# Kernel tuning notes

Hardware: AMD Instinct MI355X
Metric: run time of the kernel (lower is better)

Reference implementation:

```python
import jax, jax.numpy as jnp
import numpy as np

NUM_HEADS = 16
ROPE_THETA = 10000.0


def _rope(x, cos, sin):
    # x: [B, H, S, d_k]; cos/sin: [S, d_k//2]
    x2 = x.reshape(x.shape[:-1] + (x.shape[-1] // 2, 2))
    x0, x1 = x2[..., 0], x2[..., 1]
    out0 = cos * x0 - sin * x1
    out1 = sin * x0 + cos * x1
    return jnp.stack([out0, out1], axis=-1).reshape(x.shape)


def setup_inputs() -> dict:
    key = jax.random.key(0)
    ks = jax.random.split(key, 5)
    B, S, D = 4, 2048, 1024
    std = float(np.sqrt(2.0 / (D * D)))
    return {
        "x": jax.random.normal(ks[0], (B, S, D), dtype=jnp.float32),
        "WQ": jax.random.normal(ks[1], (D, D), dtype=jnp.float32) * std,
        "WK": jax.random.normal(ks[2], (D, D), dtype=jnp.float32) * std,
        "WV": jax.random.normal(ks[3], (D, D), dtype=jnp.float32) * std,
        "WO": jax.random.normal(ks[4], (D, D), dtype=jnp.float32) * std,
    }


def reference(x, WQ, WK, WV, WO):
    B, S, D = x.shape
    H = NUM_HEADS
    dk = D // H

    def split_heads(t):  # [B, S, D] -> [B, H, S, dk]
        return t.reshape(B, S, H, dk).transpose(0, 2, 1, 3)

    # Projections: stored weights are [out, in], applied as x @ W.T
    Q = split_heads(x @ WQ.T)
    K = split_heads(x @ WK.T)
    V = split_heads(x @ WV.T)

    # RoPE (interleaved pairs, rotation matrix formulation)
    pos = jnp.arange(S, dtype=jnp.float32)[:, None]               # [S, 1]
    dims = jnp.arange(dk // 2, dtype=jnp.float32)[None, :]        # [1, dk/2]
    thetas = pos / (ROPE_THETA ** (2.0 * dims / dk))              # [S, dk/2]
    cos, sin = jnp.cos(thetas), jnp.sin(thetas)
    Q = _rope(Q, cos, sin)
    K = _rope(K, cos, sin)

    # Causal scaled dot-product attention (full score matrix, per original)
    scores = jnp.einsum('bhqd,bhkd->bhqk', Q, K) / jnp.sqrt(jnp.float32(dk))
    mask = jnp.tril(jnp.ones((S, S), dtype=bool))                 # [S, S]
    scores = jnp.where(mask, scores, -jnp.inf)
    attn = jax.nn.softmax(scores, axis=-1)
    out = jnp.einsum('bhqk,bhkd->bhqd', attn, V)                  # [B, H, S, dk]

    merged = out.transpose(0, 2, 1, 3).reshape(B, S, D)
    return merged @ WO.T
```

## Files before the change

kernel.cpp:

```cpp
#include <hip/hip_runtime.h>
#include <stdint.h>


typedef __attribute__((ext_vector_type(8))) __bf16 bf16x8;
typedef __attribute__((ext_vector_type(4))) float f32x4;

typedef __attribute__((address_space(1))) uint32_t AS1u32;
typedef __attribute__((address_space(3))) uint32_t AS3u32;

__device__ __forceinline__ unsigned short f2bf(float f) {
  uint32_t u = __builtin_bit_cast(uint32_t, f);
  u += 0x7fffu + ((u >> 16) & 1u);
  return (unsigned short)(u >> 16);
}
__device__ __forceinline__ float bf2f(unsigned short h) {
  return __builtin_bit_cast(float, (uint32_t)h << 16);
}
__device__ __forceinline__ void lds_load16(const void* g, void* l) {
  __builtin_amdgcn_global_load_lds((AS1u32*)g, (AS3u32*)l, 16, 0, 0);
}
__device__ __forceinline__ f32x4 mfma16(bf16x8 a, bf16x8 b, f32x4 c) {
  return __builtin_amdgcn_mfma_f32_16x16x32_bf16(a, b, c, 0, 0, 0);
}

__global__ void cast_f32_to_bf16x4(const float4* __restrict__ in,
                                   uint2* __restrict__ out, int n4) {
  int i = blockIdx.x * 256 + threadIdx.x;
  if (i >= n4) return;
  float4 v = in[i];
  uint2 o;
  o.x = (uint32_t)f2bf(v.x) | ((uint32_t)f2bf(v.y) << 16);
  o.y = (uint32_t)f2bf(v.z) | ((uint32_t)f2bf(v.w) << 16);
  out[i] = o;
}

__global__ void rope_table_kernel(float* __restrict__ tab) {
  int i = blockIdx.x * 256 + threadIdx.x;
  int s = i >> 5, p = i & 31;
  double ang = (double)s * pow(10000.0, -(double)p / 32.0);
  tab[2 * i]     = (float)cos(ang);
  tab[2 * i + 1] = (float)sin(ang);
}

__global__ void rope_apply_kernel(unsigned short* __restrict__ buf,
                                  const float2* __restrict__ tab, float scale) {
  int i = blockIdx.x * 256 + threadIdx.x;
  int row = i >> 9;
  int pp  = i & 511;
  float2 cs = tab[(row & 2047) * 32 + (pp & 31)];
  uint32_t v = *(uint32_t*)(buf + 2 * (size_t)i);
  float x0 = bf2f((unsigned short)(v & 0xffffu));
  float x1 = bf2f((unsigned short)(v >> 16));
  float o0 = (cs.x * x0 - cs.y * x1) * scale;
  float o1 = (cs.y * x0 + cs.x * x1) * scale;
  *(uint32_t*)(buf + 2 * (size_t)i) =
      (uint32_t)f2bf(o0) | ((uint32_t)f2bf(o1) << 16);
}

template <int MODE>
__global__ __launch_bounds__(256)
void gemm_bt(const unsigned short* __restrict__ A,
             const unsigned short* __restrict__ B,
             unsigned short* __restrict__ Qo,
             unsigned short* __restrict__ Ko,
             unsigned short* __restrict__ Vt,
             float* __restrict__ CF,
             int M, int N, int K) {
  __shared__ unsigned short As[128 * 64];
  __shared__ unsigned short Bs[128 * 64];
  const int tid = threadIdx.x;
  const int lane = tid & 63, wave = tid >> 6;
  const int l16 = lane & 15, g4 = lane >> 4;
  const int wr = wave >> 1, wc = wave & 1;
  const int row0 = blockIdx.y * 128;
  const int col0 = blockIdx.x * 128;

  const f32x4 fz = {0.f, 0.f, 0.f, 0.f};
  f32x4 acc[4][4];
#pragma unroll
  for (int m = 0; m < 4; ++m)
#pragma unroll
    for (int n = 0; n < 4; ++n) acc[m][n] = fz;

  for (int kt = 0; kt < K; kt += 64) {
    __syncthreads();
#pragma unroll
    for (int i = 0; i < 4; ++i) {
      int flat = i * 2048 + tid * 8;
      int r = flat >> 6, c = flat & 63;
      lds_load16(A + (size_t)(row0 + r) * K + kt + c, &As[flat]);
      lds_load16(B + (size_t)(col0 + r) * K + kt + c, &Bs[flat]);
    }
    __syncthreads();
#pragma unroll
    for (int kk = 0; kk < 2; ++kk) {
      bf16x8 af[4], bfr[4];
#pragma unroll
      for (int m = 0; m < 4; ++m)
        af[m] = *(const bf16x8*)&As[(wr * 64 + m * 16 + l16) * 64 + kk * 32 + g4 * 8];
#pragma unroll
      for (int n = 0; n < 4; ++n)
        bfr[n] = *(const bf16x8*)&Bs[(wc * 64 + n * 16 + l16) * 64 + kk * 32 + g4 * 8];
#pragma unroll
      for (int m = 0; m < 4; ++m)
#pragma unroll
        for (int n = 0; n < 4; ++n)
          acc[m][n] = mfma16(af[m], bfr[n], acc[m][n]);
    }
  }

  const int rbase = row0 + wr * 64 + g4 * 4;
  const int cbase = col0 + wc * 64 + l16;
  if (MODE == 1) {
#pragma unroll
    for (int m = 0; m < 4; ++m)
#pragma unroll
      for (int n = 0; n < 4; ++n)
#pragma unroll
        for (int r = 0; r < 4; ++r)
          CF[(size_t)(rbase + m * 16 + r) * N + cbase + n * 16] = acc[m][n][r];
  } else {
    const int seg = col0 >> 10;
    if (seg < 2) {
      unsigned short* O = seg ? Ko : Qo;
      const int cl = cbase - (seg << 10);
#pragma unroll
      for (int m = 0; m < 4; ++m)
#pragma unroll
        for (int n = 0; n < 4; ++n)
#pragma unroll
          for (int r = 0; r < 4; ++r)
            O[(size_t)(rbase + m * 16 + r) * 1024 + cl + n * 16] = f2bf(acc[m][n][r]);
    } else {
#pragma unroll
      for (int m = 0; m < 4; ++m) {
        const int srow = rbase + m * 16;
        const int b = srow >> 11, s = srow & 2047;
#pragma unroll
        for (int n = 0; n < 4; ++n) {
          const int cg = cbase - 2048 + n * 16;
          const int h = cg >> 6, d = cg & 63;
          ushort4 pk;
          pk.x = f2bf(acc[m][n][0]);
          pk.y = f2bf(acc[m][n][1]);
          pk.z = f2bf(acc[m][n][2]);
          pk.w = f2bf(acc[m][n][3]);
          *(ushort4*)(Vt + ((size_t)(b * 16 + h) * 64 + d) * 2048 + s) = pk;
        }
      }
    }
  }
}

__device__ __forceinline__ void attn_step(
    const unsigned short* Ksb, const unsigned short* Vsb, unsigned short* Psw,
    const bf16x8& q0, const bf16x8& q1, float* mrow, float* lrow,
    f32x4* acc, int qrbase, bool diag, int kt,
    int l16, int g4, int c0, int x7, int pr7) {
  const f32x4 fz = {0.f, 0.f, 0.f, 0.f};

  f32x4 sc[4];
  __builtin_amdgcn_s_setprio(1);
#pragma unroll
  for (int n = 0; n < 4; ++n) {
    f32x4 s = fz;
    s = mfma16(q0, *(const bf16x8*)&Ksb[(n * 16 + l16) * 64 + c0], s);
    s = mfma16(q1, *(const bf16x8*)&Ksb[(n * 16 + l16) * 64 + (c0 ^ 32)], s);
    sc[n] = s;
  }
  __builtin_amdgcn_s_setprio(0);

  if (diag) {
#pragma unroll
    for (int n = 0; n < 4; ++n) {
      int kc = kt * 64 + n * 16 + l16;
#pragma unroll
      for (int r = 0; r < 4; ++r)
        if (kc > qrbase + r) sc[n][r] = -1e30f;
    }
  }

  float p[4][4];
#pragma unroll
  for (int r = 0; r < 4; ++r) {
    float rm = fmaxf(fmaxf(sc[0][r], sc[1][r]), fmaxf(sc[2][r], sc[3][r]));
    rm = fmaxf(rm, __shfl_xor(rm, 1));
    rm = fmaxf(rm, __shfl_xor(rm, 2));
    rm = fmaxf(rm, __shfl_xor(rm, 4));
    rm = fmaxf(rm, __shfl_xor(rm, 8));
    float mn = fmaxf(mrow[r], rm);
    float so = __builtin_amdgcn_exp2f(mrow[r] - mn);
    float sum = 0.f;
#pragma unroll
    for (int n = 0; n < 4; ++n) {
      float pv = __builtin_amdgcn_exp2f(sc[n][r] - mn);
      p[n][r] = pv;
      sum += pv;
    }
    sum += __shfl_xor(sum, 1);
    sum += __shfl_xor(sum, 2);
    sum += __shfl_xor(sum, 4);
    sum += __shfl_xor(sum, 8);
    lrow[r] = lrow[r] * so + sum;
    mrow[r] = mn;
#pragma unroll
    for (int d = 0; d < 4; ++d) acc[d][r] *= so;
  }

#pragma unroll
  for (int n = 0; n < 4; ++n) {
    int chunkbase = 2 * n + (l16 >> 3);
#pragma unroll
    for (int r = 0; r < 4; ++r) {
      int ch = chunkbase ^ (r + pr7);
      Psw[(g4 * 4 + r) * 64 + ch * 8 + x7] = f2bf(p[n][r]);
    }
  }
  bf16x8 pf0 = *(const bf16x8*)&Psw[l16 * 64 + c0];
  bf16x8 pf1 = *(const bf16x8*)&Psw[l16 * 64 + (c0 ^ 32)];

  __builtin_amdgcn_s_setprio(1);
#pragma unroll
  for (int d = 0; d < 4; ++d) {
    acc[d] = mfma16(pf0, *(const bf16x8*)&Vsb[(d * 16 + l16) * 64 + c0], acc[d]);
    acc[d] = mfma16(pf1, *(const bf16x8*)&Vsb[(d * 16 + l16) * 64 + (c0 ^ 32)], acc[d]);
  }
  __builtin_amdgcn_s_setprio(0);
}

__global__ __launch_bounds__(256)
void attn_kernel(const unsigned short* __restrict__ Qb,
                 const unsigned short* __restrict__ Kb,
                 const unsigned short* __restrict__ Vt,
                 unsigned short* __restrict__ AO) {
  __shared__ unsigned short Ks[2][64 * 64];
  __shared__ unsigned short Vs[2][64 * 64];
  __shared__ unsigned short Ps[4][16 * 64];
  const int tid = threadIdx.x;
  const int lane = tid & 63, wave = tid >> 6;
  const int l16 = lane & 15, g4 = lane >> 4;
  const int qa = blockIdx.x, qb = 31 - qa;
  const int bh = blockIdx.y;
  const int b = bh >> 4, h = bh & 15;

  const unsigned short* qpa =
      Qb + (size_t)(b * 2048 + qa * 64 + wave * 16 + l16) * 1024 + h * 64 + g4 * 8;
  const unsigned short* qpb =
      Qb + (size_t)(b * 2048 + qb * 64 + wave * 16 + l16) * 1024 + h * 64 + g4 * 8;
  const bf16x8 qfa0 = *(const bf16x8*)qpa, qfa1 = *(const bf16x8*)(qpa + 32);
  const bf16x8 qfb0 = *(const bf16x8*)qpb, qfb1 = *(const bf16x8*)(qpb + 32);

  const unsigned short* kptr[2];
  const unsigned short* vptr[2];
#pragma unroll
  for (int i = 0; i < 2; ++i) {
    int L = i * 256 + tid;
    int r = L >> 3, ch = L & 7;
    int sc8 = ((ch ^ (r & 7)) << 3);
    kptr[i] = Kb + ((size_t)b * 2048 + r) * 1024 + h * 64 + sc8;
    vptr[i] = Vt + ((size_t)bh * 64 + r) * 2048 + sc8;
  }

  const f32x4 fz = {0.f, 0.f, 0.f, 0.f};
  f32x4 acc_a[4], acc_b[4];
#pragma unroll
  for (int d = 0; d < 4; ++d) { acc_a[d] = fz; acc_b[d] = fz; }
  float ma[4], la[4], mb[4], lb[4];
#pragma unroll
  for (int r = 0; r < 4; ++r) {
    ma[r] = -1e30f; mb[r] = -1e30f; la[r] = 0.f; lb[r] = 0.f;
  }

  const int qra  = qa * 64 + wave * 16 + g4 * 4;
  const int qrb_ = qb * 64 + wave * 16 + g4 * 4;
  const int x7 = l16 & 7;
  const int c0 = (g4 ^ x7) << 3;
  const int pr7 = 4 * (g4 & 1);

#pragma unroll
  for (int i = 0; i < 2; ++i) {
    lds_load16(kptr[i], &Ks[0][(i * 256 + tid) * 8]);
    lds_load16(vptr[i], &Vs[0][(i * 256 + tid) * 8]);
  }
  __syncthreads();

  int cur = 0;
  for (int kt = 0; kt <= qb; ++kt) {
    if (kt < qb) {
#pragma unroll
      for (int i = 0; i < 2; ++i) {
        lds_load16(kptr[i] + (size_t)(kt + 1) * 65536, &Ks[cur ^ 1][(i * 256 + tid) * 8]);
        lds_load16(vptr[i] + (size_t)(kt + 1) * 64,    &Vs[cur ^ 1][(i * 256 + tid) * 8]);
      }
    }
    attn_step(Ks[cur], Vs[cur], Ps[wave], qfb0, qfb1, mb, lb, acc_b, qrb_,
              kt == qb, kt, l16, g4, c0, x7, pr7);
    if (kt <= qa)
      attn_step(Ks[cur], Vs[cur], Ps[wave], qfa0, qfa1, ma, la, acc_a, qra,
                kt == qa, kt, l16, g4, c0, x7, pr7);
    __syncthreads();
    cur ^= 1;
  }

  {
    const size_t ob = (size_t)(b * 2048 + qb * 64 + wave * 16 + g4 * 4) * 1024 + h * 64 + l16;
#pragma unroll
    for (int r = 0; r < 4; ++r) {
      float inv = 1.f / lb[r];
#pragma unroll
      for (int d = 0; d < 4; ++d)
        AO[ob + (size_t)r * 1024 + d * 16] = f2bf(acc_b[d][r] * inv);
    }
  }
  {
    const size_t ob = (size_t)(b * 2048 + qa * 64 + wave * 16 + g4 * 4) * 1024 + h * 64 + l16;
#pragma unroll
    for (int r = 0; r < 4; ++r) {
      float inv = 1.f / la[r];
#pragma unroll
      for (int d = 0; d < 4; ++d)
        AO[ob + (size_t)r * 1024 + d * 16] = f2bf(acc_a[d][r] * inv);
    }
  }
}

extern "C" void kernel_launch(void* const* d_in, const int* in_sizes, int n_in,
                              void* d_out, int out_size, void* d_ws, size_t ws_size,
                              hipStream_t stream) {
  const float* x  = (const float*)d_in[0];
  const float* WQ = (const float*)d_in[1];
  const float* WK = (const float*)d_in[2];
  const float* WV = (const float*)d_in[3];
  const float* WO = (const float*)d_in[4];
  float* out = (float*)d_out;

  unsigned short* xb   = (unsigned short*)d_ws;
  unsigned short* wqkv = xb + (size_t)8192 * 1024;
  unsigned short* wo   = wqkv + (size_t)3072 * 1024;
  unsigned short* Qb   = wo + (size_t)1024 * 1024;
  unsigned short* Kb   = Qb + (size_t)8192 * 1024;
  unsigned short* Vt   = Kb + (size_t)8192 * 1024;
  float* tab = (float*)(Vt + (size_t)8192 * 1024);

  cast_f32_to_bf16x4<<<8192, 256, 0, stream>>>((const float4*)x, (uint2*)xb, 8192 * 1024 / 4);
  cast_f32_to_bf16x4<<<1024, 256, 0, stream>>>((const float4*)WQ, (uint2*)wqkv, 1024 * 1024 / 4);
  cast_f32_to_bf16x4<<<1024, 256, 0, stream>>>((const float4*)WK, (uint2*)(wqkv + (size_t)1024 * 1024), 1024 * 1024 / 4);
  cast_f32_to_bf16x4<<<1024, 256, 0, stream>>>((const float4*)WV, (uint2*)(wqkv + (size_t)2048 * 1024), 1024 * 1024 / 4);
  cast_f32_to_bf16x4<<<1024, 256, 0, stream>>>((const float4*)WO, (uint2*)wo, 1024 * 1024 / 4);
  rope_table_kernel<<<256, 256, 0, stream>>>(tab);

  gemm_bt<0><<<dim3(24, 64), 256, 0, stream>>>(xb, wqkv, Qb, Kb, Vt, nullptr, 8192, 3072, 1024);

  rope_apply_kernel<<<16384, 256, 0, stream>>>(Qb, (const float2*)tab, 0.18033688011112042f);
  rope_apply_kernel<<<16384, 256, 0, stream>>>(Kb, (const float2*)tab, 1.0f);

  attn_kernel<<<dim3(16, 64), 256, 0, stream>>>(Qb, Kb, Vt, xb);

  gemm_bt<1><<<dim3(8, 64), 256, 0, stream>>>(xb, wo, nullptr, nullptr, nullptr, out, 8192, 1024, 1024);
}
```

Baseline: 364.7 us.

## Merge cast and RoPE launches; use lazy softmax rescale and MFMA row sums

Merges the five cast kernels into one launch and the two RoPE apply kernels into one 2D launch, cutting launch overhead. In attention, the running max is updated and the accumulators rescaled only when some row's new max exceeds the old one by more than a threshold. The softmax denominator is computed by an extra MFMA against a ones vector instead of shuffle reductions. This removes shuffle and exp work per step, but computes the denominator from bf16-rounded probabilities and lets exponents grow up to 2^8 before rescaling.

New measurement: 359.9 us. About the same (-1.3%).

```diff
diff --git a/kernel.cpp b/kernel.cpp
--- a/kernel.cpp
+++ b/kernel.cpp
@@ -23,15 +23,28 @@
   return __builtin_amdgcn_mfma_f32_16x16x32_bf16(a, b, c, 0, 0, 0);
 }
 
-__global__ void cast_f32_to_bf16x4(const float4* __restrict__ in,
-                                   uint2* __restrict__ out, int n4) {
-  int i = blockIdx.x * 256 + threadIdx.x;
-  if (i >= n4) return;
-  float4 v = in[i];
+__global__ void cast_all_kernel(const float4* __restrict__ x,
+                                const float4* __restrict__ wq,
+                                const float4* __restrict__ wk,
+                                const float4* __restrict__ wv,
+                                const float4* __restrict__ wo_in,
+                                uint2* __restrict__ xb,
+                                uint2* __restrict__ wqkv,
+                                uint2* __restrict__ wo_out) {
+  const int bid = blockIdx.x;
+  const float4* src;
+  uint2* dst;
+  int idx;
+  if (bid < 8192)       { src = x;     dst = xb;             idx = bid * 256 + threadIdx.x; }
+  else if (bid < 9216)  { src = wq;    dst = wqkv;           idx = (bid - 8192) * 256 + threadIdx.x; }
+  else if (bid < 10240) { src = wk;    dst = wqkv + 262144;  idx = (bid - 9216) * 256 + threadIdx.x; }
+  else if (bid < 11264) { src = wv;    dst = wqkv + 524288;  idx = (bid - 10240) * 256 + threadIdx.x; }
+  else                  { src = wo_in; dst = wo_out;         idx = (bid - 11264) * 256 + threadIdx.x; }
+  float4 v = src[idx];
   uint2 o;
   o.x = (uint32_t)f2bf(v.x) | ((uint32_t)f2bf(v.y) << 16);
   o.y = (uint32_t)f2bf(v.z) | ((uint32_t)f2bf(v.w) << 16);
-  out[i] = o;
+  dst[idx] = o;
 }
 
 __global__ void rope_table_kernel(float* __restrict__ tab) {
@@ -42,8 +55,11 @@
   tab[2 * i + 1] = (float)sin(ang);
 }
 
-__global__ void rope_apply_kernel(unsigned short* __restrict__ buf,
-                                  const float2* __restrict__ tab, float scale) {
+__global__ void rope_apply_kernel(unsigned short* __restrict__ Qb,
+                                  unsigned short* __restrict__ Kb,
+                                  const float2* __restrict__ tab) {
+  unsigned short* buf = blockIdx.y ? Kb : Qb;
+  const float scale = blockIdx.y ? 1.0f : 0.18033688011112042f;
   int i = blockIdx.x * 256 + threadIdx.x;
   int row = i >> 9;
   int pp  = i & 511;
@@ -154,8 +170,8 @@
 
 __device__ __forceinline__ void attn_step(
     const unsigned short* Ksb, const unsigned short* Vsb, unsigned short* Psw,
-    const bf16x8& q0, const bf16x8& q1, float* mrow, float* lrow,
-    f32x4* acc, int qrbase, bool diag, int kt,
+    const bf16x8& q0, const bf16x8& q1, float* mrow, f32x4& acc_l,
+    f32x4* acc, const bf16x8& ones8, int qrbase, bool diag, int kt,
     int l16, int g4, int c0, int x7, int pr7) {
   const f32x4 fz = {0.f, 0.f, 0.f, 0.f};
 
@@ -188,23 +204,17 @@
     rm = fmaxf(rm, __shfl_xor(rm, 2));
     rm = fmaxf(rm, __shfl_xor(rm, 4));
     rm = fmaxf(rm, __shfl_xor(rm, 8));
-    float mn = fmaxf(mrow[r], rm);
-    float so = __builtin_amdgcn_exp2f(mrow[r] - mn);
-    float sum = 0.f;
-#pragma unroll
-    for (int n = 0; n < 4; ++n) {
-      float pv = __builtin_amdgcn_exp2f(sc[n][r] - mn);
-      p[n][r] = pv;
-      sum += pv;
-    }
-    sum += __shfl_xor(sum, 1);
-    sum += __shfl_xor(sum, 2);
-    sum += __shfl_xor(sum, 4);
-    sum += __shfl_xor(sum, 8);
-    lrow[r] = lrow[r] * so + sum;
-    mrow[r] = mn;
-#pragma unroll
-    for (int d = 0; d < 4; ++d) acc[d][r] *= so;
+    if (!__all(rm <= mrow[r] + 8.f)) {
+      float mn = fmaxf(mrow[r], rm);
+      float so = __builtin_amdgcn_exp2f(mrow[r] - mn);
+      acc_l[r] *= so;
+#pragma unroll
+      for (int d = 0; d < 4; ++d) acc[d][r] *= so;
+      mrow[r] = mn;
+    }
+#pragma unroll
+    for (int n = 0; n < 4; ++n)
+      p[n][r] = __builtin_amdgcn_exp2f(sc[n][r] - mrow[r]);
   }
 
 #pragma unroll
@@ -220,6 +230,8 @@
   bf16x8 pf1 = *(const bf16x8*)&Psw[l16 * 64 + (c0 ^ 32)];
 
   __builtin_amdgcn_s_setprio(1);
+  acc_l = mfma16(pf0, ones8, acc_l);
+  acc_l = mfma16(pf1, ones8, acc_l);
 #pragma unroll
   for (int d = 0; d < 4; ++d) {
     acc[d] = mfma16(pf0, *(const bf16x8*)&Vsb[(d * 16 + l16) * 64 + c0], acc[d]);
@@ -262,14 +274,12 @@
   }
 
   const f32x4 fz = {0.f, 0.f, 0.f, 0.f};
-  f32x4 acc_a[4], acc_b[4];
+  f32x4 acc_a[4], acc_b[4], acc_la = fz, acc_lb = fz;
 #pragma unroll
   for (int d = 0; d < 4; ++d) { acc_a[d] = fz; acc_b[d] = fz; }
-  float ma[4], la[4], mb[4], lb[4];
-#pragma unroll
-  for (int r = 0; r < 4; ++r) {
-    ma[r] = -1e30f; mb[r] = -1e30f; la[r] = 0.f; lb[r] = 0.f;
-  }
+  float ma[4], mb[4];
+#pragma unroll
+  for (int r = 0; r < 4; ++r) { ma[r] = -1e30f; mb[r] = -1e30f; }
 
   const int qra  = qa * 64 + wave * 16 + g4 * 4;
   const int qrb_ = qb * 64 + wave * 16 + g4 * 4;
@@ -277,6 +287,10 @@
   const int c0 = (g4 ^ x7) << 3;
   const int pr7 = 4 * (g4 & 1);
 
+  bf16x8 ones8;
+#pragma unroll
+  for (int j = 0; j < 8; ++j) ones8[j] = (__bf16)1.0f;
+
 #pragma unroll
   for (int i = 0; i < 2; ++i) {
     lds_load16(kptr[i], &Ks[0][(i * 256 + tid) * 8]);
@@ -293,11 +307,11 @@
         lds_load16(vptr[i] + (size_t)(kt + 1) * 64,    &Vs[cur ^ 1][(i * 256 + tid) * 8]);
       }
     }
-    attn_step(Ks[cur], Vs[cur], Ps[wave], qfb0, qfb1, mb, lb, acc_b, qrb_,
-              kt == qb, kt, l16, g4, c0, x7, pr7);
+    attn_step(Ks[cur], Vs[cur], Ps[wave], qfb0, qfb1, mb, acc_lb, acc_b, ones8,
+              qrb_, kt == qb, kt, l16, g4, c0, x7, pr7);
     if (kt <= qa)
-      attn_step(Ks[cur], Vs[cur], Ps[wave], qfa0, qfa1, ma, la, acc_a, qra,
-                kt == qa, kt, l16, g4, c0, x7, pr7);
+      attn_step(Ks[cur], Vs[cur], Ps[wave], qfa0, qfa1, ma, acc_la, acc_a, ones8,
+                qra, kt == qa, kt, l16, g4, c0, x7, pr7);
     __syncthreads();
     cur ^= 1;
   }
@@ -306,7 +320,7 @@
     const size_t ob = (size_t)(b * 2048 + qb * 64 + wave * 16 + g4 * 4) * 1024 + h * 64 + l16;
 #pragma unroll
     for (int r = 0; r < 4; ++r) {
-      float inv = 1.f / lb[r];
+      float inv = 1.f / acc_lb[r];
 #pragma unroll
       for (int d = 0; d < 4; ++d)
         AO[ob + (size_t)r * 1024 + d * 16] = f2bf(acc_b[d][r] * inv);
@@ -316,7 +330,7 @@
     const size_t ob = (size_t)(b * 2048 + qa * 64 + wave * 16 + g4 * 4) * 1024 + h * 64 + l16;
 #pragma unroll
     for (int r = 0; r < 4; ++r) {
-      float inv = 1.f / la[r];
+      float inv = 1.f / acc_la[r];
 #pragma unroll
       for (int d = 0; d < 4; ++d)
         AO[ob + (size_t)r * 1024 + d * 16] = f2bf(acc_a[d][r] * inv);
@@ -342,17 +356,15 @@
   unsigned short* Vt   = Kb + (size_t)8192 * 1024;
   float* tab = (float*)(Vt + (size_t)8192 * 1024);
 
-  cast_f32_to_bf16x4<<<8192, 256, 0, stream>>>((const float4*)x, (uint2*)xb, 8192 * 1024 / 4);
-  cast_f32_to_bf16x4<<<1024, 256, 0, stream>>>((const float4*)WQ, (uint2*)wqkv, 1024 * 1024 / 4);
-  cast_f32_to_bf16x4<<<1024, 256, 0, stream>>>((const float4*)WK, (uint2*)(wqkv + (size_t)1024 * 1024), 1024 * 1024 / 4);
-  cast_f32_to_bf16x4<<<1024, 256, 0, stream>>>((const float4*)WV, (uint2*)(wqkv + (size_t)2048 * 1024), 1024 * 1024 / 4);
-  cast_f32_to_bf16x4<<<1024, 256, 0, stream>>>((const float4*)WO, (uint2*)wo, 1024 * 1024 / 4);
+  cast_all_kernel<<<12288, 256, 0, stream>>>(
+      (const float4*)x, (const float4*)WQ, (const float4*)WK,
+      (const float4*)WV, (const float4*)WO,
+      (uint2*)xb, (uint2*)wqkv, (uint2*)wo);
   rope_table_kernel<<<256, 256, 0, stream>>>(tab);
 
   gemm_bt<0><<<dim3(24, 64), 256, 0, stream>>>(xb, wqkv, Qb, Kb, Vt, nullptr, 8192, 3072, 1024);
 
-  rope_apply_kernel<<<16384, 256, 0, stream>>>(Qb, (const float2*)tab, 0.18033688011112042f);
-  rope_apply_kernel<<<16384, 256, 0, stream>>>(Kb, (const float2*)tab, 1.0f);
+  rope_apply_kernel<<<dim3(16384, 2), 256, 0, stream>>>(Qb, Kb, (const float2*)tab);
 
   attn_kernel<<<dim3(16, 64), 256, 0, stream>>>(Qb, Kb, Vt, xb);
 
```
